# Kernel optimization log

Measured on AMD Instinct MI355X. Metric: run time of the kernel, lower is better.

The kernel has to match this reference:

```python
import jax, jax.numpy as jnp
import numpy as np
import math

L = 16.0
DT = 1.0
TAU = 10.0
THRESHOLD = 1.0
ALPHA = 0.01
DECAY = math.exp(-DT / TAU)

@jax.custom_vjp
def multibit_spike(x):
    # forward: floor(x) clipped to [0, L]
    return jnp.clip(jnp.floor(x), 0.0, L)

def _spike_fwd(x):
    return multibit_spike(x), x

def _spike_bwd(x, g):
    dist = jnp.abs(x - jnp.round(x))
    scale = jnp.clip(1.0 - 2.0 * dist, 0.0, 1.0)
    in_range = ((x >= 0.0) & (x <= L + 1.0)).astype(g.dtype)
    return (g * in_range * scale,)

multibit_spike.defvjp(_spike_fwd, _spike_bwd)

def setup_inputs() -> dict:
    key = jax.random.key(0)
    k_x, k_w = jax.random.split(key)
    B, T, IN, H = 16, 2048, 512, 512
    # SNN-aware init: std = 0.5*threshold / (sqrt(fan_in)*0.3)
    std = 0.5 * THRESHOLD / (math.sqrt(IN) * 0.3)
    x = jax.random.normal(k_x, (B, T, IN), dtype=jnp.float32)
    W = jax.random.normal(k_w, (H, IN), dtype=jnp.float32) * std
    b = jnp.zeros((H,), dtype=jnp.float32)
    return {"x": x, "W": W, "b": b}

def reference(x, W, b):
    B, T, _ = x.shape
    Hd = W.shape[0]
    # batched linear projection of the whole sequence (compute-heavy GEMM)
    h = jnp.einsum('bti,hi->bth', x, W) + b  # [B, T, H]
    v0 = jnp.zeros((B, Hd), dtype=x.dtype)
    theta0 = jnp.full((B, Hd), THRESHOLD, dtype=x.dtype)

    def step(carry, i_t):
        v, theta = carry
        v = v * DECAY + i_t
        clamp_limit = L * theta * 2.0
        v = jnp.clip(v, -clamp_limit, clamp_limit)
        spike = multibit_spike(v / theta)
        v = v - spike * theta
        theta = theta + ALPHA * spike - ALPHA * (theta - THRESHOLD)
        return (v, theta), spike

    (v_f, theta_f), spikes_tbh = jax.lax.scan(step, (v0, theta0), jnp.swapaxes(h, 0, 1))
    spikes = jnp.swapaxes(spikes_tbh, 0, 1)  # [B, T, H]
    return spikes, v_f, theta_f
```

## Files before the change

### kernel.cpp

```cpp
#include <hip/hip_runtime.h>

#define B_  16
#define T_  2048
#define IN_ 512
#define H_  512
#define M_  (B_ * T_)

static __device__ __forceinline__ float4 ld4(const float* p) {
    return *reinterpret_cast<const float4*>(p);
}

#define BM 128
#define BN 128
#define BK 16
#define LDT (BM + 4)

__global__ __launch_bounds__(256)
void gemm_xwT(const float* __restrict__ X, const float* __restrict__ W,
              const float* __restrict__ bias, float* __restrict__ Hout) {
    __shared__ float As[BK][LDT];
    __shared__ float Bs[BK][LDT];

    const int tid = threadIdx.x;
    const int m0  = blockIdx.x * BM;
    const int n0  = blockIdx.y * BN;

    const int tx = tid & 15;
    const int ty = tid >> 4;

    const int row = tid >> 2;
    const int kph = (tid & 3) * 4;

    float acc[8][8];
#pragma unroll
    for (int i = 0; i < 8; ++i)
#pragma unroll
        for (int j = 0; j < 8; ++j) acc[i][j] = 0.0f;

    for (int k0 = 0; k0 < IN_; k0 += BK) {
        float4 a0 = ld4(&X[(size_t)(m0 + row)      * IN_ + k0 + kph]);
        float4 a1 = ld4(&X[(size_t)(m0 + row + 64) * IN_ + k0 + kph]);
        float4 b0 = ld4(&W[(size_t)(n0 + row)      * IN_ + k0 + kph]);
        float4 b1 = ld4(&W[(size_t)(n0 + row + 64) * IN_ + k0 + kph]);

        As[kph + 0][row]      = a0.x;  As[kph + 1][row]      = a0.y;
        As[kph + 2][row]      = a0.z;  As[kph + 3][row]      = a0.w;
        As[kph + 0][row + 64] = a1.x;  As[kph + 1][row + 64] = a1.y;
        As[kph + 2][row + 64] = a1.z;  As[kph + 3][row + 64] = a1.w;
        Bs[kph + 0][row]      = b0.x;  Bs[kph + 1][row]      = b0.y;
        Bs[kph + 2][row]      = b0.z;  Bs[kph + 3][row]      = b0.w;
        Bs[kph + 0][row + 64] = b1.x;  Bs[kph + 1][row + 64] = b1.y;
        Bs[kph + 2][row + 64] = b1.z;  Bs[kph + 3][row + 64] = b1.w;
        __syncthreads();

#pragma unroll
        for (int k = 0; k < BK; ++k) {
            float4 av0 = ld4(&As[k][ty * 8]);
            float4 av1 = ld4(&As[k][ty * 8 + 4]);
            float4 bv0 = ld4(&Bs[k][tx * 8]);
            float4 bv1 = ld4(&Bs[k][tx * 8 + 4]);
            const float am[8] = {av0.x, av0.y, av0.z, av0.w,
                                 av1.x, av1.y, av1.z, av1.w};
            const float bn8[8] = {bv0.x, bv0.y, bv0.z, bv0.w,
                                  bv1.x, bv1.y, bv1.z, bv1.w};
#pragma unroll
            for (int i = 0; i < 8; ++i)
#pragma unroll
                for (int j = 0; j < 8; ++j)
                    acc[i][j] = fmaf(am[i], bn8[j], acc[i][j]);
        }
        __syncthreads();
    }

    float4 bb0 = ld4(&bias[n0 + tx * 8]);
    float4 bb1 = ld4(&bias[n0 + tx * 8 + 4]);
#pragma unroll
    for (int i = 0; i < 8; ++i) {
        const int rowo = m0 + ty * 8 + i;
        float4 o0, o1;
        o0.x = acc[i][0] + bb0.x;  o0.y = acc[i][1] + bb0.y;
        o0.z = acc[i][2] + bb0.z;  o0.w = acc[i][3] + bb0.w;
        o1.x = acc[i][4] + bb1.x;  o1.y = acc[i][5] + bb1.y;
        o1.z = acc[i][6] + bb1.z;  o1.w = acc[i][7] + bb1.w;
        *reinterpret_cast<float4*>(&Hout[(size_t)rowo * H_ + n0 + tx * 8])     = o0;
        *reinterpret_cast<float4*>(&Hout[(size_t)rowo * H_ + n0 + tx * 8 + 4]) = o1;
    }
}

#define PF 16

__global__ __launch_bounds__(64)
void gif_scan(const float* __restrict__ Hbuf, float* __restrict__ spikes,
              float* __restrict__ vout, float* __restrict__ thout) {
    const int gid = blockIdx.x * 64 + threadIdx.x;
    const int b = gid >> 9;
    const int h = gid & 511;

    const float* ip = Hbuf   + (size_t)b * T_ * H_ + h;
    float*       sp = spikes + (size_t)b * T_ * H_ + h;

    const float DECAY_F = 0.9048374180359595f;
    const float ALPHA_F = 0.01f;

    float buf[PF];
#pragma unroll
    for (int j = 0; j < PF; ++j) buf[j] = ip[(size_t)j * H_];

    float v = 0.0f, theta = 1.0f;
    for (int t0 = 0; t0 < T_; t0 += PF) {
        float nbuf[PF];
        const int tnx = t0 + PF;
        if (tnx < T_) {
#pragma unroll
            for (int j = 0; j < PF; ++j) nbuf[j] = ip[(size_t)(tnx + j) * H_];
        }
#pragma unroll
        for (int j = 0; j < PF; ++j) {
            float cur = buf[j];
            v = v * DECAY_F + cur;
            float cl = 32.0f * theta;
            v = fminf(fmaxf(v, -cl), cl);
            float s = floorf(v / theta);
            s = fminf(fmaxf(s, 0.0f), 16.0f);
            v = v - s * theta;
            theta = theta + ALPHA_F * s - ALPHA_F * (theta - 1.0f);
            sp[(size_t)(t0 + j) * H_] = s;
        }
#pragma unroll
        for (int j = 0; j < PF; ++j) buf[j] = nbuf[j];
    }
    vout[gid]  = v;
    thout[gid] = theta;
}

extern "C" void kernel_launch(void* const* d_in, const int* in_sizes, int n_in,
                              void* d_out, int out_size, void* d_ws, size_t ws_size,
                              hipStream_t stream) {
    const float* x    = (const float*)d_in[0];
    const float* W    = (const float*)d_in[1];
    const float* bias = (const float*)d_in[2];

    float* out   = (float*)d_out;
    float* hbuf  = (float*)d_ws;

    float* spikes = out;
    float* v_f    = out + (size_t)B_ * T_ * H_;
    float* th_f   = v_f + (size_t)B_ * H_;

    dim3 grid(M_ / BM, H_ / BN);
    gemm_xwT<<<grid, 256, 0, stream>>>(x, W, bias, hbuf);
    gif_scan<<<(B_ * H_) / 64, 64, 0, stream>>>(hbuf, spikes, v_f, th_f);
}
```

Before: 442.4 us.

## Prefetch GEMM tiles into registers, interleave fragment layout, retune scan kernel

The GEMM now loads the next K-slice of X and W into registers while the current shared-memory tile is being consumed, so global-load latency overlaps with the FMA loop. Each thread's 8x8 output is split into two 4-wide halves 64 apart, which changes the shared-memory read pattern to reduce bank conflicts. The scan kernel doubles its prefetch depth, uses 256-thread blocks, and replaces the IEEE divide with a reciprocal plus Newton refinement. The extra registers raise register pressure, the larger blocks mean only 32 workgroups for the scan, and the refined reciprocal must match floor(v/theta) exactly near integer boundaries.

Result: faster. 408.5 us (-7.7%).

```diff
diff --git a/kernel.cpp b/kernel.cpp
--- a/kernel.cpp
+++ b/kernel.cpp
@@ -6,14 +6,14 @@
 #define H_  512
 #define M_  (B_ * T_)
 
-static __device__ __forceinline__ float4 ld4(const float* p) {
-    return *reinterpret_cast<const float4*>(p);
-}
-
 #define BM 128
 #define BN 128
 #define BK 16
 #define LDT (BM + 4)
+
+static __device__ __forceinline__ float4 ld4(const float* p) {
+    return *reinterpret_cast<const float4*>(p);
+}
 
 __global__ __launch_bounds__(256)
 void gemm_xwT(const float* __restrict__ X, const float* __restrict__ W,
@@ -31,6 +31,13 @@
     const int row = tid >> 2;
     const int kph = (tid & 3) * 4;
 
+    const float* pa0 = X + (size_t)(m0 + row) * IN_ + kph;
+    const float* pa1 = pa0 + (size_t)64 * IN_;
+    const float* pb0 = W + (size_t)(n0 + row) * IN_ + kph;
+    const float* pb1 = pb0 + (size_t)64 * IN_;
+
+    float4 ra0 = ld4(pa0), ra1 = ld4(pa1), rb0 = ld4(pb0), rb1 = ld4(pb1);
+
     float acc[8][8];
 #pragma unroll
     for (int i = 0; i < 8; ++i)
@@ -38,27 +45,27 @@
         for (int j = 0; j < 8; ++j) acc[i][j] = 0.0f;
 
     for (int k0 = 0; k0 < IN_; k0 += BK) {
-        float4 a0 = ld4(&X[(size_t)(m0 + row)      * IN_ + k0 + kph]);
-        float4 a1 = ld4(&X[(size_t)(m0 + row + 64) * IN_ + k0 + kph]);
-        float4 b0 = ld4(&W[(size_t)(n0 + row)      * IN_ + k0 + kph]);
-        float4 b1 = ld4(&W[(size_t)(n0 + row + 64) * IN_ + k0 + kph]);
+        As[kph + 0][row]      = ra0.x;  As[kph + 1][row]      = ra0.y;
+        As[kph + 2][row]      = ra0.z;  As[kph + 3][row]      = ra0.w;
+        As[kph + 0][row + 64] = ra1.x;  As[kph + 1][row + 64] = ra1.y;
+        As[kph + 2][row + 64] = ra1.z;  As[kph + 3][row + 64] = ra1.w;
+        Bs[kph + 0][row]      = rb0.x;  Bs[kph + 1][row]      = rb0.y;
+        Bs[kph + 2][row]      = rb0.z;  Bs[kph + 3][row]      = rb0.w;
+        Bs[kph + 0][row + 64] = rb1.x;  Bs[kph + 1][row + 64] = rb1.y;
+        Bs[kph + 2][row + 64] = rb1.z;  Bs[kph + 3][row + 64] = rb1.w;
+        __syncthreads();
 
-        As[kph + 0][row]      = a0.x;  As[kph + 1][row]      = a0.y;
-        As[kph + 2][row]      = a0.z;  As[kph + 3][row]      = a0.w;
-        As[kph + 0][row + 64] = a1.x;  As[kph + 1][row + 64] = a1.y;
-        As[kph + 2][row + 64] = a1.z;  As[kph + 3][row + 64] = a1.w;
-        Bs[kph + 0][row]      = b0.x;  Bs[kph + 1][row]      = b0.y;
-        Bs[kph + 2][row]      = b0.z;  Bs[kph + 3][row]      = b0.w;
-        Bs[kph + 0][row + 64] = b1.x;  Bs[kph + 1][row + 64] = b1.y;
-        Bs[kph + 2][row + 64] = b1.z;  Bs[kph + 3][row + 64] = b1.w;
-        __syncthreads();
+        if (k0 + BK < IN_) {
+            ra0 = ld4(pa0 + k0 + BK);  ra1 = ld4(pa1 + k0 + BK);
+            rb0 = ld4(pb0 + k0 + BK);  rb1 = ld4(pb1 + k0 + BK);
+        }
 
 #pragma unroll
         for (int k = 0; k < BK; ++k) {
-            float4 av0 = ld4(&As[k][ty * 8]);
-            float4 av1 = ld4(&As[k][ty * 8 + 4]);
-            float4 bv0 = ld4(&Bs[k][tx * 8]);
-            float4 bv1 = ld4(&Bs[k][tx * 8 + 4]);
+            float4 av0 = ld4(&As[k][ty * 4]);
+            float4 av1 = ld4(&As[k][ty * 4 + 64]);
+            float4 bv0 = ld4(&Bs[k][tx * 4]);
+            float4 bv1 = ld4(&Bs[k][tx * 4 + 64]);
             const float am[8] = {av0.x, av0.y, av0.z, av0.w,
                                  av1.x, av1.y, av1.z, av1.w};
             const float bn8[8] = {bv0.x, bv0.y, bv0.z, bv0.w,
@@ -72,27 +79,27 @@
         __syncthreads();
     }
 
-    float4 bb0 = ld4(&bias[n0 + tx * 8]);
-    float4 bb1 = ld4(&bias[n0 + tx * 8 + 4]);
+    float4 bb0 = ld4(&bias[n0 + tx * 4]);
+    float4 bb1 = ld4(&bias[n0 + tx * 4 + 64]);
 #pragma unroll
     for (int i = 0; i < 8; ++i) {
-        const int rowo = m0 + ty * 8 + i;
+        const int r = m0 + ((i < 4) ? (ty * 4 + i) : (64 + ty * 4 + (i - 4)));
         float4 o0, o1;
         o0.x = acc[i][0] + bb0.x;  o0.y = acc[i][1] + bb0.y;
         o0.z = acc[i][2] + bb0.z;  o0.w = acc[i][3] + bb0.w;
         o1.x = acc[i][4] + bb1.x;  o1.y = acc[i][5] + bb1.y;
         o1.z = acc[i][6] + bb1.z;  o1.w = acc[i][7] + bb1.w;
-        *reinterpret_cast<float4*>(&Hout[(size_t)rowo * H_ + n0 + tx * 8])     = o0;
-        *reinterpret_cast<float4*>(&Hout[(size_t)rowo * H_ + n0 + tx * 8 + 4]) = o1;
+        *reinterpret_cast<float4*>(&Hout[(size_t)r * H_ + n0 + tx * 4])      = o0;
+        *reinterpret_cast<float4*>(&Hout[(size_t)r * H_ + n0 + tx * 4 + 64]) = o1;
     }
 }
 
-#define PF 16
+#define PF 32
 
-__global__ __launch_bounds__(64)
+__global__ __launch_bounds__(256)
 void gif_scan(const float* __restrict__ Hbuf, float* __restrict__ spikes,
               float* __restrict__ vout, float* __restrict__ thout) {
-    const int gid = blockIdx.x * 64 + threadIdx.x;
+    const int gid = blockIdx.x * 256 + threadIdx.x;
     const int b = gid >> 9;
     const int h = gid & 511;
 
@@ -120,7 +127,17 @@
             v = v * DECAY_F + cur;
             float cl = 32.0f * theta;
             v = fminf(fmaxf(v, -cl), cl);
-            float s = floorf(v / theta);
+
+            float r0 = __builtin_amdgcn_rcpf(theta);
+            float e0 = fmaf(-theta, r0, 1.0f);
+            float r1 = fmaf(r0, e0, r0);
+            float e1 = fmaf(-theta, r1, 1.0f);
+            float r2 = fmaf(r1, e1, r1);
+            float q0 = v * r2;
+            float er = fmaf(-theta, q0, v);
+            float q  = fmaf(er, r2, q0);
+
+            float s = floorf(q);
             s = fminf(fmaxf(s, 0.0f), 16.0f);
             v = v - s * theta;
             theta = theta + ALPHA_F * s - ALPHA_F * (theta - 1.0f);
@@ -140,14 +157,14 @@
     const float* W    = (const float*)d_in[1];
     const float* bias = (const float*)d_in[2];
 
-    float* out   = (float*)d_out;
-    float* hbuf  = (float*)d_ws;
+    float* out    = (float*)d_out;
+    float* spikes = out;
+    float* v_f    = out + (size_t)M_ * H_;
+    float* th_f   = v_f + (size_t)B_ * H_;
 
-    float* spikes = out;
-    float* v_f    = out + (size_t)B_ * T_ * H_;
-    float* th_f   = v_f + (size_t)B_ * H_;
+    float* hbuf   = (float*)d_ws;
 
     dim3 grid(M_ / BM, H_ / BN);
     gemm_xwT<<<grid, 256, 0, stream>>>(x, W, bias, hbuf);
-    gif_scan<<<(B_ * H_) / 64, 64, 0, stream>>>(hbuf, spikes, v_f, th_f);
+    gif_scan<<<(B_ * H_) / 256, 256, 0, stream>>>(hbuf, spikes, v_f, th_f);
 }
```
